# Optimization experiments

Measured on AMD Instinct MI355X. Metric: run time of the kernel, lower is better.

Reference implementation:

```python
import jax, jax.numpy as jnp
import numpy as np

N = 20000       # num_nodes
E = 640000      # num_edges
LATENT = 64
HIDDEN = 128
NFEAT = 64
NEG_SLOPE = 0.2


def _gat_conv(x, src, dst, W, a_s, a_d, b):
    """Single-head GAT layer. x: [N, Fin]; W: [Fout, Fin]; a_s, a_d, b: [Fout]."""
    h = x @ W.T                                   # [N, Fout]
    # per-node attention logits, gathered per edge
    e = jax.nn.leaky_relu((h @ a_s)[src] + (h @ a_d)[dst], NEG_SLOPE)  # [E]
    # segment softmax over incoming edges of each target node
    m = jax.ops.segment_max(e, dst, num_segments=N)                    # [N]
    ex = jnp.exp(e - m[dst])                                           # [E]
    s = jax.ops.segment_sum(ex, dst, num_segments=N)                   # [N]
    alpha = ex / (s[dst] + 1e-16)                                      # [E]
    out = jax.ops.segment_sum(h[src] * alpha[:, None], dst, num_segments=N)  # [N, Fout]
    return out + b


def setup_inputs() -> dict:
    key = jax.random.key(0)
    ks = jax.random.split(key, 16)
    g = lambda k, shp, sc: (jax.random.normal(k, shp, dtype=jnp.float32) * sc)
    return {
        "z": g(ks[0], (LATENT,), 1.0),
        "edge_index": jax.random.randint(ks[1], (2, E), 0, N, dtype=jnp.int64 if jax.config.jax_enable_x64 else jnp.int32),
        "fc_w": g(ks[2], (N * LATENT, LATENT), 0.05),
        "fc_b": g(ks[3], (N * LATENT,), 0.05),
        "W0": g(ks[4], (HIDDEN, LATENT), 0.05),
        "as0": g(ks[5], (HIDDEN,), 0.05),
        "ad0": g(ks[6], (HIDDEN,), 0.05),
        "b0": jnp.zeros((HIDDEN,), jnp.float32),
        "W1": g(ks[7], (HIDDEN, HIDDEN), 0.05),
        "as1": g(ks[8], (HIDDEN,), 0.05),
        "ad1": g(ks[9], (HIDDEN,), 0.05),
        "b1": jnp.zeros((HIDDEN,), jnp.float32),
        "W2": g(ks[10], (NFEAT, HIDDEN), 0.05),
        "as2": g(ks[11], (NFEAT,), 0.05),
        "ad2": g(ks[12], (NFEAT,), 0.05),
        "b2": jnp.zeros((NFEAT,), jnp.float32),
    }


def reference(z, edge_index, fc_w, fc_b, W0, as0, ad0, b0, W1, as1, ad1, b1, W2, as2, ad2, b2):
    src, dst = edge_index[0], edge_index[1]
    # latent -> per-node features
    x = jax.nn.relu(z @ fc_w.T + fc_b).reshape(N, LATENT)
    x = jax.nn.relu(_gat_conv(x, src, dst, W0, as0, ad0, b0))
    x = jax.nn.relu(_gat_conv(x, src, dst, W1, as1, ad1, b1))
    x = _gat_conv(x, src, dst, W2, as2, ad2, b2)   # [N, NFEAT], no relu on last
    return x
```

## Files before the change

kernel.cpp:

```cpp
#include <hip/hip_runtime.h>

#define NEG_SLOPE 0.2f

typedef __attribute__((ext_vector_type(8))) short short8;
typedef __attribute__((ext_vector_type(4))) float v4f;

__device__ __forceinline__ float wave_red_sum(float v) {
    for (int o = 32; o > 0; o >>= 1) v += __shfl_xor(v, o, 64);
    return v;
}
__device__ __forceinline__ float wave_red_max(float v) {
    for (int o = 32; o > 0; o >>= 1) v = fmaxf(v, __shfl_xor(v, o, 64));
    return v;
}
__device__ __forceinline__ unsigned short f2bf(float f) {
    union { float f; unsigned int u; } x; x.f = f;
    unsigned int r = x.u + 0x7fffu + ((x.u >> 16) & 1u);
    return (unsigned short)(r >> 16);
}
__device__ __forceinline__ float bf2f(unsigned short b) {
    union { unsigned int u; float f; } x; x.u = ((unsigned int)b) << 16;
    return x.f;
}
__device__ __forceinline__ void split_bf(float v, unsigned short& hi, unsigned short& lo) {
    hi = f2bf(v);
    lo = f2bf(v - bf2f(hi));
}

__global__ void fc_kernel(const float* __restrict__ z, const float* __restrict__ fcw,
                          const float* __restrict__ fcb, unsigned short* __restrict__ xhi,
                          unsigned short* __restrict__ xlo, int R) {
    int t = blockIdx.x * 256 + threadIdx.x;
    int r = t >> 4;
    int j = t & 15;
    if (r >= R) return;
    float4 wz = ((const float4*)z)[j];
    float4 ww = ((const float4*)fcw)[r * 16 + j];
    float p = wz.x * ww.x + wz.y * ww.y + wz.z * ww.z + wz.w * ww.w;
    p += __shfl_xor(p, 1, 64);
    p += __shfl_xor(p, 2, 64);
    p += __shfl_xor(p, 4, 64);
    p += __shfl_xor(p, 8, 64);
    if (j == 0) {
        float v = p + fcb[r];
        v = v > 0.f ? v : 0.f;
        unsigned short hi, lo;
        split_bf(v, hi, lo);
        xhi[r] = hi;
        xlo[r] = lo;
    }
}

__global__ void wsplit_kernel(const float* __restrict__ W0, const float* __restrict__ W1,
                              const float* __restrict__ W2, int n0, int n1, int n2,
                              unsigned short* __restrict__ whi, unsigned short* __restrict__ wlo) {
    int i = blockIdx.x * 256 + threadIdx.x;
    if (i >= n0 + n1 + n2) return;
    float v;
    if (i < n0) v = W0[i];
    else if (i < n0 + n1) v = W1[i - n0];
    else v = W2[i - n0 - n1];
    unsigned short hi, lo;
    split_bf(v, hi, lo);
    whi[i] = hi;
    wlo[i] = lo;
}

template <int FIN, int FOUT>
__global__ __launch_bounds__(256) void gemm_att_kernel(
        const unsigned short* __restrict__ xhi, const unsigned short* __restrict__ xlo,
        const unsigned short* __restrict__ whi, const unsigned short* __restrict__ wlo,
        const float* __restrict__ as, const float* __restrict__ ad,
        float* __restrict__ h, float* __restrict__ hs, float* __restrict__ hd, int Mtiles) {
    constexpr int NT = FOUT / 16;
    constexpr int KS = FIN / 32;
    const int wid = blockIdx.x * 4 + (threadIdx.x >> 6);
    if (wid >= Mtiles) return;
    const int lane = threadIdx.x & 63;
    const int l15 = lane & 15;
    const int quad = lane >> 4;
    const int v0 = wid * 16;

    v4f acc[NT];
#pragma unroll
    for (int nt = 0; nt < NT; nt++) acc[nt] = (v4f){0.f, 0.f, 0.f, 0.f};

    const unsigned short* xh = xhi + (v0 + l15) * FIN + quad * 8;
    const unsigned short* xl = xlo + (v0 + l15) * FIN + quad * 8;
    const unsigned short* wh = whi + l15 * FIN + quad * 8;
    const unsigned short* wl = wlo + l15 * FIN + quad * 8;
#pragma unroll
    for (int ks = 0; ks < KS; ks++) {
        short8 ah = *(const short8*)(xh + ks * 32);
        short8 al = *(const short8*)(xl + ks * 32);
#pragma unroll
        for (int nt = 0; nt < NT; nt++) {
            short8 bh = *(const short8*)(wh + nt * 16 * FIN + ks * 32);
            short8 bl = *(const short8*)(wl + nt * 16 * FIN + ks * 32);
            acc[nt] = __builtin_amdgcn_mfma_f32_16x16x32_bf16(ah, bh, acc[nt], 0, 0, 0);
            acc[nt] = __builtin_amdgcn_mfma_f32_16x16x32_bf16(ah, bl, acc[nt], 0, 0, 0);
            acc[nt] = __builtin_amdgcn_mfma_f32_16x16x32_bf16(al, bh, acc[nt], 0, 0, 0);
        }
    }
    float ps[4] = {0.f, 0.f, 0.f, 0.f}, pd[4] = {0.f, 0.f, 0.f, 0.f};
#pragma unroll
    for (int nt = 0; nt < NT; nt++) {
        float av = as[nt * 16 + l15];
        float dv = ad[nt * 16 + l15];
#pragma unroll
        for (int r = 0; r < 4; r++) {
            float c = acc[nt][r];
            h[(v0 + quad * 4 + r) * FOUT + nt * 16 + l15] = c;
            ps[r] += c * av;
            pd[r] += c * dv;
        }
    }
#pragma unroll
    for (int o = 8; o >= 1; o >>= 1) {
#pragma unroll
        for (int r = 0; r < 4; r++) {
            ps[r] += __shfl_xor(ps[r], o, 64);
            pd[r] += __shfl_xor(pd[r], o, 64);
        }
    }
    if (l15 == 0) {
#pragma unroll
        for (int r = 0; r < 4; r++) {
            hs[v0 + quad * 4 + r] = ps[r];
            hd[v0 + quad * 4 + r] = pd[r];
        }
    }
}

__global__ void hist_kernel(const int* __restrict__ dst, int* __restrict__ cnt, int E) {
    int e = blockIdx.x * 256 + threadIdx.x;
    if (e < E) atomicAdd(&cnt[dst[e]], 1);
}

__global__ void scan1_kernel(const int* __restrict__ cnt, int* __restrict__ rowtmp,
                             int* __restrict__ bsum) {
    __shared__ int sd[256];
    int i = blockIdx.x * 256 + threadIdx.x;
    sd[threadIdx.x] = cnt[i];
    for (int off = 1; off < 256; off <<= 1) {
        __syncthreads();
        int t = (threadIdx.x >= off) ? sd[threadIdx.x - off] : 0;
        __syncthreads();
        sd[threadIdx.x] += t;
    }
    __syncthreads();
    rowtmp[i] = sd[threadIdx.x];
    if (threadIdx.x == 255) bsum[blockIdx.x] = sd[255];
}

__global__ void scan2_kernel(const int* __restrict__ bsum, int* __restrict__ boff, int nb) {
    __shared__ int sd[128];
    int i = threadIdx.x;
    int orig = (i < nb) ? bsum[i] : 0;
    sd[i] = orig;
    for (int off = 1; off < 128; off <<= 1) {
        __syncthreads();
        int t = (i >= off) ? sd[i - off] : 0;
        __syncthreads();
        sd[i] += t;
    }
    __syncthreads();
    if (i < nb) boff[i] = sd[i] - orig;
}

__global__ void scan3_kernel(const int* __restrict__ cnt, const int* __restrict__ rowtmp,
                             const int* __restrict__ boff, int* __restrict__ rowptr,
                             int* __restrict__ cursor, int N) {
    int i = blockIdx.x * 256 + threadIdx.x;
    if (i > N) return;
    int b = i >> 8;
    int excl = boff[b] + rowtmp[i] - cnt[i];
    rowptr[i] = excl;
    if (i < N) cursor[i] = excl;
}

__global__ void scatter_kernel(const int* __restrict__ src, const int* __restrict__ dst,
                               int* __restrict__ cursor, int* __restrict__ col, int E) {
    int e = blockIdx.x * 256 + threadIdx.x;
    if (e < E) {
        int p = atomicAdd(&cursor[dst[e]], 1);
        col[p] = src[e];
    }
}

template <int FOUT, bool RELU, bool SPLIT>
__global__ __launch_bounds__(256) void agg_kernel(
        const float* __restrict__ h, const float* __restrict__ hs, const float* __restrict__ hd,
        const int* __restrict__ rowptr, const int* __restrict__ col, const float* __restrict__ b,
        float* __restrict__ out, unsigned short* __restrict__ ohi,
        unsigned short* __restrict__ olo) {
    constexpr int FPT = FOUT / 64;
    constexpr int CAP = 512;
    __shared__ float sw[4][CAP];
    __shared__ int ssv[4][CAP];
    const int w = threadIdx.x >> 6;
    const int lane = threadIdx.x & 63;
    const int v = blockIdx.x * 4 + w;
    float* swv = sw[w];
    int* ssvv = ssv[w];
    const int s0 = rowptr[v];
    const int deg = rowptr[v + 1] - s0;
    float acc[FPT];
#pragma unroll
    for (int i = 0; i < FPT; i++) acc[i] = 0.f;
    float inv = 0.f;
    if (deg > 0) {
        const float hdv = hd[v];
        float mt = -1e30f;
        for (int j = lane; j < deg; j += 64) {
            int sv = col[s0 + j];
            float e = hs[sv] + hdv;
            e = e > 0.f ? e : NEG_SLOPE * e;
            if (j < CAP) { ssvv[j] = sv; swv[j] = e; }
            mt = fmaxf(mt, e);
        }
        const float m = wave_red_max(mt);
        float st = 0.f;
        for (int j = lane; j < deg; j += 64) {
            float e;
            if (j < CAP) e = swv[j];
            else {
                int sv = col[s0 + j];
                e = hs[sv] + hdv;
                e = e > 0.f ? e : NEG_SLOPE * e;
            }
            float ww = __expf(e - m);
            if (j < CAP) swv[j] = ww;
            st += ww;
        }
        const float ssum = wave_red_sum(st);
        inv = 1.f / (ssum + 1e-16f);
        const int dmain = deg < CAP ? deg : CAP;
#pragma unroll 4
        for (int jj = 0; jj < dmain; jj++) {
            float ww = swv[jj];
            int sv = ssvv[jj];
            if (FPT == 2) {
                float2 hv = ((const float2*)(h + sv * FOUT))[lane];
                acc[0] += ww * hv.x;
                acc[1] += ww * hv.y;
            } else {
                acc[0] += ww * h[sv * FOUT + lane];
            }
        }
        for (int jj = CAP; jj < deg; jj++) {
            int sv = col[s0 + jj];
            float e = hs[sv] + hdv;
            e = e > 0.f ? e : NEG_SLOPE * e;
            float ww = __expf(e - m);
            if (FPT == 2) {
                float2 hv = ((const float2*)(h + sv * FOUT))[lane];
                acc[0] += ww * hv.x;
                acc[1] += ww * hv.y;
            } else {
                acc[0] += ww * h[sv * FOUT + lane];
            }
        }
    }
    float o[FPT];
#pragma unroll
    for (int i = 0; i < FPT; i++) {
        float bv = b[lane * FPT + i];
        o[i] = acc[i] * inv + bv;
        if (RELU) o[i] = fmaxf(o[i], 0.f);
    }
    if (SPLIT) {
        if (FPT == 2) {
            unsigned short h0, l0, h1, l1;
            split_bf(o[0], h0, l0);
            split_bf(o[1], h1, l1);
            ((ushort2*)ohi)[v * 64 + lane] = make_ushort2(h0, h1);
            ((ushort2*)olo)[v * 64 + lane] = make_ushort2(l0, l1);
        } else {
            unsigned short hb, lb;
            split_bf(o[0], hb, lb);
            ohi[v * FOUT + lane] = hb;
            olo[v * FOUT + lane] = lb;
        }
    } else {
        if (FPT == 2)
            ((float2*)out)[v * 64 + lane] = make_float2(o[0], o[1]);
        else
            out[v * FOUT + lane] = o[0];
    }
}

extern "C" void kernel_launch(void* const* d_in, const int* in_sizes, int n_in,
                              void* d_out, int out_size, void* d_ws, size_t ws_size,
                              hipStream_t stream) {
    const float* z   = (const float*)d_in[0];
    const int*   ei  = (const int*)d_in[1];
    const float* fcw = (const float*)d_in[2];
    const float* fcb = (const float*)d_in[3];
    const float* W0  = (const float*)d_in[4];
    const float* as0 = (const float*)d_in[5];
    const float* ad0 = (const float*)d_in[6];
    const float* b0  = (const float*)d_in[7];
    const float* W1  = (const float*)d_in[8];
    const float* as1 = (const float*)d_in[9];
    const float* ad1 = (const float*)d_in[10];
    const float* b1  = (const float*)d_in[11];
    const float* W2  = (const float*)d_in[12];
    const float* as2 = (const float*)d_in[13];
    const float* ad2 = (const float*)d_in[14];
    const float* b2  = (const float*)d_in[15];

    const int E = in_sizes[1] / 2;
    const int R = in_sizes[3];
    const int N = R / 64;
    const int n0 = in_sizes[4];
    const int n1 = in_sizes[8];
    const int n2 = in_sizes[12];
    const int* src = ei;
    const int* dst = ei + E;

    char* p = (char*)d_ws;
    auto carve = [&](size_t bytes) {
        void* r = (void*)p;
        p += (bytes + 255) & ~(size_t)255;
        return r;
    };
    unsigned short* xhi = (unsigned short*)carve((size_t)N * 128 * 2);
    unsigned short* xlo = (unsigned short*)carve((size_t)N * 128 * 2);
    float* hbuf = (float*)carve((size_t)N * 128 * 4);
    float* hs = (float*)carve((size_t)N * 4);
    float* hd = (float*)carve((size_t)N * 4);
    unsigned short* whi = (unsigned short*)carve((size_t)(n0 + n1 + n2) * 2);
    unsigned short* wlo = (unsigned short*)carve((size_t)(n0 + n1 + n2) * 2);
    const int nb = (N + 255) / 256;
    int* cnt = (int*)carve((size_t)nb * 256 * 4);
    int* rowtmp = (int*)carve((size_t)nb * 256 * 4);
    int* rowptr = (int*)carve((size_t)(N + 32) * 4);
    int* cursor = (int*)carve((size_t)N * 4);
    int* bsum = (int*)carve(128 * 4);
    int* boff = (int*)carve(128 * 4);
    int* col = (int*)carve((size_t)E * 4);

    hipMemsetAsync(cnt, 0, (size_t)nb * 256 * 4, stream);
    hist_kernel<<<(E + 255) / 256, 256, 0, stream>>>(dst, cnt, E);
    scan1_kernel<<<nb, 256, 0, stream>>>(cnt, rowtmp, bsum);
    scan2_kernel<<<1, 128, 0, stream>>>(bsum, boff, nb);
    scan3_kernel<<<(N + 256) / 256, 256, 0, stream>>>(cnt, rowtmp, boff, rowptr, cursor, N);
    scatter_kernel<<<(E + 255) / 256, 256, 0, stream>>>(src, dst, cursor, col, E);

    wsplit_kernel<<<(n0 + n1 + n2 + 255) / 256, 256, 0, stream>>>(W0, W1, W2, n0, n1, n2, whi, wlo);
    fc_kernel<<<R / 16, 256, 0, stream>>>(z, fcw, fcb, xhi, xlo, R);

    const int Mtiles = N / 16;
    const int gblocks = (Mtiles + 3) / 4;

    gemm_att_kernel<64, 128><<<gblocks, 256, 0, stream>>>(xhi, xlo, whi, wlo, as0, ad0,
                                                          hbuf, hs, hd, Mtiles);
    agg_kernel<128, true, true><<<N / 4, 256, 0, stream>>>(hbuf, hs, hd, rowptr, col, b0,
                                                           nullptr, xhi, xlo);
    gemm_att_kernel<128, 128><<<gblocks, 256, 0, stream>>>(xhi, xlo, whi + n0, wlo + n0, as1, ad1,
                                                           hbuf, hs, hd, Mtiles);
    agg_kernel<128, true, true><<<N / 4, 256, 0, stream>>>(hbuf, hs, hd, rowptr, col, b1,
                                                           nullptr, xhi, xlo);
    gemm_att_kernel<128, 64><<<gblocks, 256, 0, stream>>>(xhi, xlo, whi + n0 + n1, wlo + n0 + n1,
                                                          as2, ad2, hbuf, hs, hd, Mtiles);
    agg_kernel<64, false, false><<<N / 4, 256, 0, stream>>>(hbuf, hs, hd, rowptr, col, b2,
                                                            (float*)d_out, nullptr, nullptr);
}
```

Baseline: 670.0 us.

## Merge preprocessing kernels, use single-block scan, overlap CSR scatter with first GEMM

Combines the FC, degree histogram and weight-split kernels into one launch and replaces the three-pass prefix scan with a single 1024-thread block scan. The CSR scatter is merged into the same launch as the first GEMM+attention kernel so the two independent jobs share one grid. It also lowers the aggregation shared-memory edge cache from 512 to 128 entries and raises the inner-loop unroll, trading more spill-path work on high-degree nodes for higher occupancy. The aim is to cut launch count and serialization in the fixed setup phase.

```diff
diff --git a/kernel.cpp b/kernel.cpp
--- a/kernel.cpp
+++ b/kernel.cpp
@@ -27,56 +27,96 @@
     lo = f2bf(v - bf2f(hi));
 }
 
-__global__ void fc_kernel(const float* __restrict__ z, const float* __restrict__ fcw,
-                          const float* __restrict__ fcb, unsigned short* __restrict__ xhi,
-                          unsigned short* __restrict__ xlo, int R) {
-    int t = blockIdx.x * 256 + threadIdx.x;
-    int r = t >> 4;
-    int j = t & 15;
-    if (r >= R) return;
-    float4 wz = ((const float4*)z)[j];
-    float4 ww = ((const float4*)fcw)[r * 16 + j];
-    float p = wz.x * ww.x + wz.y * ww.y + wz.z * ww.z + wz.w * ww.w;
-    p += __shfl_xor(p, 1, 64);
-    p += __shfl_xor(p, 2, 64);
-    p += __shfl_xor(p, 4, 64);
-    p += __shfl_xor(p, 8, 64);
-    if (j == 0) {
-        float v = p + fcb[r];
-        v = v > 0.f ? v : 0.f;
+__global__ __launch_bounds__(256) void mega1_kernel(
+        const float* __restrict__ z, const float* __restrict__ fcw, const float* __restrict__ fcb,
+        unsigned short* __restrict__ xhi, unsigned short* __restrict__ xlo, int R, int FB,
+        const int* __restrict__ dst, int* __restrict__ cnt, int E, int HB,
+        const float* __restrict__ W0, const float* __restrict__ W1, const float* __restrict__ W2,
+        int n0, int n1, int n2, unsigned short* __restrict__ whi, unsigned short* __restrict__ wlo) {
+    const int b = blockIdx.x;
+    if (b < FB) {
+        int t = b * 256 + threadIdx.x;
+        int r = t >> 4;
+        int j = t & 15;
+        if (r >= R) return;
+        float4 wz = ((const float4*)z)[j];
+        float4 ww = ((const float4*)fcw)[r * 16 + j];
+        float p = wz.x * ww.x + wz.y * ww.y + wz.z * ww.z + wz.w * ww.w;
+        p += __shfl_xor(p, 1, 64);
+        p += __shfl_xor(p, 2, 64);
+        p += __shfl_xor(p, 4, 64);
+        p += __shfl_xor(p, 8, 64);
+        if (j == 0) {
+            float v = p + fcb[r];
+            v = v > 0.f ? v : 0.f;
+            unsigned short hi, lo;
+            split_bf(v, hi, lo);
+            xhi[r] = hi;
+            xlo[r] = lo;
+        }
+    } else if (b < FB + HB) {
+        int e = (b - FB) * 256 + threadIdx.x;
+        if (e < E) atomicAdd(&cnt[dst[e]], 1);
+    } else {
+        int i = (b - FB - HB) * 256 + threadIdx.x;
+        int ntot = n0 + n1 + n2;
+        if (i >= ntot) return;
+        float v;
+        if (i < n0) v = W0[i];
+        else if (i < n0 + n1) v = W1[i - n0];
+        else v = W2[i - n0 - n1];
         unsigned short hi, lo;
         split_bf(v, hi, lo);
-        xhi[r] = hi;
-        xlo[r] = lo;
-    }
-}
-
-__global__ void wsplit_kernel(const float* __restrict__ W0, const float* __restrict__ W1,
-                              const float* __restrict__ W2, int n0, int n1, int n2,
-                              unsigned short* __restrict__ whi, unsigned short* __restrict__ wlo) {
-    int i = blockIdx.x * 256 + threadIdx.x;
-    if (i >= n0 + n1 + n2) return;
-    float v;
-    if (i < n0) v = W0[i];
-    else if (i < n0 + n1) v = W1[i - n0];
-    else v = W2[i - n0 - n1];
-    unsigned short hi, lo;
-    split_bf(v, hi, lo);
-    whi[i] = hi;
-    wlo[i] = lo;
+        whi[i] = hi;
+        wlo[i] = lo;
+    }
+}
+
+__global__ __launch_bounds__(1024) void scan_kernel(const int* __restrict__ cnt,
+                                                    int* __restrict__ rowptr,
+                                                    int* __restrict__ cursor, int N) {
+    constexpr int CH = 20;
+    __shared__ int wsum[16];
+    const int t = threadIdx.x;
+    const int lane = t & 63, wid = t >> 6;
+    const int base = t * CH;
+    int loc[CH];
+    int s = 0;
+#pragma unroll
+    for (int i = 0; i < CH; i++) {
+        int idx = base + i;
+        loc[i] = (idx < N) ? cnt[idx] : 0;
+        s += loc[i];
+    }
+    int v = s;
+    for (int off = 1; off < 64; off <<= 1) {
+        int n = __shfl_up(v, off, 64);
+        if (lane >= off) v += n;
+    }
+    if (lane == 63) wsum[wid] = v;
+    __syncthreads();
+    int woff = 0;
+    for (int i = 0; i < wid; i++) woff += wsum[i];
+    int excl = woff + v - s;
+#pragma unroll
+    for (int i = 0; i < CH; i++) {
+        int idx = base + i;
+        if (idx < N) { rowptr[idx] = excl; cursor[idx] = excl; }
+        excl += loc[i];
+    }
+    if (t == 1023) rowptr[N] = excl;
 }
 
 template <int FIN, int FOUT>
-__global__ __launch_bounds__(256) void gemm_att_kernel(
-        const unsigned short* __restrict__ xhi, const unsigned short* __restrict__ xlo,
-        const unsigned short* __restrict__ whi, const unsigned short* __restrict__ wlo,
-        const float* __restrict__ as, const float* __restrict__ ad,
-        float* __restrict__ h, float* __restrict__ hs, float* __restrict__ hd, int Mtiles) {
+__device__ __forceinline__ void gemm_att_body(
+        int wid, int lane, const unsigned short* __restrict__ xhi,
+        const unsigned short* __restrict__ xlo, const unsigned short* __restrict__ whi,
+        const unsigned short* __restrict__ wlo, const float* __restrict__ as,
+        const float* __restrict__ ad, float* __restrict__ h, float* __restrict__ hs,
+        float* __restrict__ hd, int Mtiles) {
     constexpr int NT = FOUT / 16;
     constexpr int KS = FIN / 32;
-    const int wid = blockIdx.x * 4 + (threadIdx.x >> 6);
     if (wid >= Mtiles) return;
-    const int lane = threadIdx.x & 63;
     const int l15 = lane & 15;
     const int quad = lane >> 4;
     const int v0 = wid * 16;
@@ -132,59 +172,32 @@
     }
 }
 
-__global__ void hist_kernel(const int* __restrict__ dst, int* __restrict__ cnt, int E) {
-    int e = blockIdx.x * 256 + threadIdx.x;
-    if (e < E) atomicAdd(&cnt[dst[e]], 1);
-}
-
-__global__ void scan1_kernel(const int* __restrict__ cnt, int* __restrict__ rowtmp,
-                             int* __restrict__ bsum) {
-    __shared__ int sd[256];
-    int i = blockIdx.x * 256 + threadIdx.x;
-    sd[threadIdx.x] = cnt[i];
-    for (int off = 1; off < 256; off <<= 1) {
-        __syncthreads();
-        int t = (threadIdx.x >= off) ? sd[threadIdx.x - off] : 0;
-        __syncthreads();
-        sd[threadIdx.x] += t;
-    }
-    __syncthreads();
-    rowtmp[i] = sd[threadIdx.x];
-    if (threadIdx.x == 255) bsum[blockIdx.x] = sd[255];
-}
-
-__global__ void scan2_kernel(const int* __restrict__ bsum, int* __restrict__ boff, int nb) {
-    __shared__ int sd[128];
-    int i = threadIdx.x;
-    int orig = (i < nb) ? bsum[i] : 0;
-    sd[i] = orig;
-    for (int off = 1; off < 128; off <<= 1) {
-        __syncthreads();
-        int t = (i >= off) ? sd[i - off] : 0;
-        __syncthreads();
-        sd[i] += t;
-    }
-    __syncthreads();
-    if (i < nb) boff[i] = sd[i] - orig;
-}
-
-__global__ void scan3_kernel(const int* __restrict__ cnt, const int* __restrict__ rowtmp,
-                             const int* __restrict__ boff, int* __restrict__ rowptr,
-                             int* __restrict__ cursor, int N) {
-    int i = blockIdx.x * 256 + threadIdx.x;
-    if (i > N) return;
-    int b = i >> 8;
-    int excl = boff[b] + rowtmp[i] - cnt[i];
-    rowptr[i] = excl;
-    if (i < N) cursor[i] = excl;
-}
-
-__global__ void scatter_kernel(const int* __restrict__ src, const int* __restrict__ dst,
-                               int* __restrict__ cursor, int* __restrict__ col, int E) {
-    int e = blockIdx.x * 256 + threadIdx.x;
-    if (e < E) {
-        int p = atomicAdd(&cursor[dst[e]], 1);
-        col[p] = src[e];
+template <int FIN, int FOUT>
+__global__ __launch_bounds__(256) void gemm_att_kernel(
+        const unsigned short* __restrict__ xhi, const unsigned short* __restrict__ xlo,
+        const unsigned short* __restrict__ whi, const unsigned short* __restrict__ wlo,
+        const float* __restrict__ as, const float* __restrict__ ad, float* __restrict__ h,
+        float* __restrict__ hs, float* __restrict__ hd, int Mtiles) {
+    gemm_att_body<FIN, FOUT>(blockIdx.x * 4 + (threadIdx.x >> 6), threadIdx.x & 63, xhi, xlo,
+                             whi, wlo, as, ad, h, hs, hd, Mtiles);
+}
+
+__global__ __launch_bounds__(256) void scatter_gemm0_kernel(
+        const int* __restrict__ src, const int* __restrict__ dst, int* __restrict__ cursor,
+        int* __restrict__ col, int E, int SB,
+        const unsigned short* __restrict__ xhi, const unsigned short* __restrict__ xlo,
+        const unsigned short* __restrict__ whi, const unsigned short* __restrict__ wlo,
+        const float* __restrict__ as, const float* __restrict__ ad, float* __restrict__ h,
+        float* __restrict__ hs, float* __restrict__ hd, int Mtiles) {
+    if (blockIdx.x < SB) {
+        int e = blockIdx.x * 256 + threadIdx.x;
+        if (e < E) {
+            int p = atomicAdd(&cursor[dst[e]], 1);
+            col[p] = src[e];
+        }
+    } else {
+        gemm_att_body<64, 128>((blockIdx.x - SB) * 4 + (threadIdx.x >> 6), threadIdx.x & 63,
+                               xhi, xlo, whi, wlo, as, ad, h, hs, hd, Mtiles);
     }
 }
 
@@ -195,7 +208,7 @@
         float* __restrict__ out, unsigned short* __restrict__ ohi,
         unsigned short* __restrict__ olo) {
     constexpr int FPT = FOUT / 64;
-    constexpr int CAP = 512;
+    constexpr int CAP = 128;
     __shared__ float sw[4][CAP];
     __shared__ int ssv[4][CAP];
     const int w = threadIdx.x >> 6;
@@ -236,7 +249,7 @@
         const float ssum = wave_red_sum(st);
         inv = 1.f / (ssum + 1e-16f);
         const int dmain = deg < CAP ? deg : CAP;
-#pragma unroll 4
+#pragma unroll 8
         for (int jj = 0; jj < dmain; jj++) {
             float ww = swv[jj];
             int sv = ssvv[jj];
@@ -332,38 +345,34 @@
     float* hd = (float*)carve((size_t)N * 4);
     unsigned short* whi = (unsigned short*)carve((size_t)(n0 + n1 + n2) * 2);
     unsigned short* wlo = (unsigned short*)carve((size_t)(n0 + n1 + n2) * 2);
-    const int nb = (N + 255) / 256;
-    int* cnt = (int*)carve((size_t)nb * 256 * 4);
-    int* rowtmp = (int*)carve((size_t)nb * 256 * 4);
+    int* cnt = (int*)carve((size_t)N * 4);
     int* rowptr = (int*)carve((size_t)(N + 32) * 4);
     int* cursor = (int*)carve((size_t)N * 4);
-    int* bsum = (int*)carve(128 * 4);
-    int* boff = (int*)carve(128 * 4);
     int* col = (int*)carve((size_t)E * 4);
 
-    hipMemsetAsync(cnt, 0, (size_t)nb * 256 * 4, stream);
-    hist_kernel<<<(E + 255) / 256, 256, 0, stream>>>(dst, cnt, E);
-    scan1_kernel<<<nb, 256, 0, stream>>>(cnt, rowtmp, bsum);
-    scan2_kernel<<<1, 128, 0, stream>>>(bsum, boff, nb);
-    scan3_kernel<<<(N + 256) / 256, 256, 0, stream>>>(cnt, rowtmp, boff, rowptr, cursor, N);
-    scatter_kernel<<<(E + 255) / 256, 256, 0, stream>>>(src, dst, cursor, col, E);
-
-    wsplit_kernel<<<(n0 + n1 + n2 + 255) / 256, 256, 0, stream>>>(W0, W1, W2, n0, n1, n2, whi, wlo);
-    fc_kernel<<<R / 16, 256, 0, stream>>>(z, fcw, fcb, xhi, xlo, R);
-
+    const int FB = R / 16;
+    const int HB = (E + 255) / 256;
+    const int WB = (n0 + n1 + n2 + 255) / 256;
     const int Mtiles = N / 16;
-    const int gblocks = (Mtiles + 3) / 4;
-
-    gemm_att_kernel<64, 128><<<gblocks, 256, 0, stream>>>(xhi, xlo, whi, wlo, as0, ad0,
-                                                          hbuf, hs, hd, Mtiles);
+    const int GB = (Mtiles + 3) / 4;
+    const int SB = (E + 255) / 256;
+
+    hipMemsetAsync(cnt, 0, (size_t)N * 4, stream);
+    mega1_kernel<<<FB + HB + WB, 256, 0, stream>>>(z, fcw, fcb, xhi, xlo, R, FB,
+                                                   dst, cnt, E, HB,
+                                                   W0, W1, W2, n0, n1, n2, whi, wlo);
+    scan_kernel<<<1, 1024, 0, stream>>>(cnt, rowptr, cursor, N);
+    scatter_gemm0_kernel<<<SB + GB, 256, 0, stream>>>(src, dst, cursor, col, E, SB,
+                                                      xhi, xlo, whi, wlo, as0, ad0,
+                                                      hbuf, hs, hd, Mtiles);
     agg_kernel<128, true, true><<<N / 4, 256, 0, stream>>>(hbuf, hs, hd, rowptr, col, b0,
                                                            nullptr, xhi, xlo);
-    gemm_att_kernel<128, 128><<<gblocks, 256, 0, stream>>>(xhi, xlo, whi + n0, wlo + n0, as1, ad1,
-                                                           hbuf, hs, hd, Mtiles);
+    gemm_att_kernel<128, 128><<<GB, 256, 0, stream>>>(xhi, xlo, whi + n0, wlo + n0, as1, ad1,
+                                                      hbuf, hs, hd, Mtiles);
     agg_kernel<128, true, true><<<N / 4, 256, 0, stream>>>(hbuf, hs, hd, rowptr, col, b1,
                                                            nullptr, xhi, xlo);
-    gemm_att_kernel<128, 64><<<gblocks, 256, 0, stream>>>(xhi, xlo, whi + n0 + n1, wlo + n0 + n1,
-                                                          as2, ad2, hbuf, hs, hd, Mtiles);
+    gemm_att_kernel<128, 64><<<GB, 256, 0, stream>>>(xhi, xlo, whi + n0 + n1, wlo + n0 + n1,
+                                                     as2, ad2, hbuf, hs, hd, Mtiles);
     agg_kernel<64, false, false><<<N / 4, 256, 0, stream>>>(hbuf, hs, hd, rowptr, col, b2,
                                                             (float*)d_out, nullptr, nullptr);
 }
```

Measured after the change: 690.0 us. 3.0% more time.
